# Optimization experiments

Hardware: AMD Instinct MI355X
Metric: run time of the kernel (lower is better)

The kernel has to match this reference:

```python
import jax, jax.numpy as jnp
import numpy as np

HIDDEN = 512
INPUT = 128
OUTPUT = 128
PRED_LEN = 32


def _gru_cell(h, gi, gh):
    # gi, gh: [B, 3H] pre-activations (input-side and hidden-side)
    i_r, i_z, i_n = jnp.split(gi, 3, axis=-1)
    h_r, h_z, h_n = jnp.split(gh, 3, axis=-1)
    r = jax.nn.sigmoid(i_r + h_r)
    z = jax.nn.sigmoid(i_z + h_z)
    n = jnp.tanh(i_n + r * h_n)
    return (1.0 - z) * n + z * h


def setup_inputs() -> dict:
    key = jax.random.key(0)
    ks = jax.random.split(key, 7)
    B, L = 512, 512
    s = 0.05
    return {
        "z_seq": jax.random.normal(ks[0], (B, L, INPUT), dtype=jnp.float32),
        "W_ih": jax.random.normal(ks[1], (3 * HIDDEN, INPUT), dtype=jnp.float32) * s,
        "W_hh": jax.random.normal(ks[2], (3 * HIDDEN, HIDDEN), dtype=jnp.float32) * s,
        "b_ih": jax.random.normal(ks[3], (3 * HIDDEN,), dtype=jnp.float32) * s,
        "b_hh": jax.random.normal(ks[4], (3 * HIDDEN,), dtype=jnp.float32) * s,
        "W_out": jax.random.normal(ks[5], (OUTPUT, HIDDEN), dtype=jnp.float32) * s,
        "b_out": jax.random.normal(ks[6], (OUTPUT,), dtype=jnp.float32) * s,
    }


def reference(z_seq, W_ih, W_hh, b_ih, b_hh, W_out, b_out):
    B, L, C = z_seq.shape
    h0 = jnp.zeros((B, HIDDEN), dtype=z_seq.dtype)

    # Precompute input-side pre-activations for all encode steps: [L, B, 3H]
    gi_enc = jnp.einsum('blc,gc->lbg', z_seq, W_ih) + b_ih

    def enc_step(h, gi):
        gh = h @ W_hh.T + b_hh
        return _gru_cell(h, gi, gh), None

    h_t, _ = jax.lax.scan(enc_step, h0, gi_enc)

    # Decode: input is always zeros, so input-side pre-activation is just b_ih
    gi_dec = jnp.broadcast_to(b_ih, (B, 3 * HIDDEN))

    def dec_step(h, _):
        gh = h @ W_hh.T + b_hh
        h_new = _gru_cell(h, gi_dec, gh)
        y = h_new @ W_out.T + b_out
        return h_new, y

    _, ys = jax.lax.scan(dec_step, h_t, None, length=PRED_LEN)  # [pred_len, B, O]
    return jnp.transpose(ys, (1, 0, 2))  # [B, pred_len, O]
```

## Files before the change

### kernel.cpp

```cpp
#include <hip/hip_runtime.h>

#define BATCH 512
#define SEQL  512
#define NIN   128
#define NH    512
#define NOUT  128
#define PRED  32
#define NSTEP (SEQL + PRED)

#define G_B 8
#define G_H 32
#define BT  64
#define NWG (G_B * G_H)
#define NTHREADS 256

#define OFF_WIH  24576
#define OFF_WOUT 30720
#define OFF_TR   38912
#define LDS_SH   40448

typedef short bf16x8 __attribute__((ext_vector_type(8)));
typedef float f32x4 __attribute__((ext_vector_type(4)));
typedef unsigned int u32x4 __attribute__((ext_vector_type(4)));

#define MFMA __builtin_amdgcn_mfma_f32_16x16x32_bf16

__device__ __forceinline__ unsigned short f2bf(float f) {
    unsigned int u = __float_as_uint(f);
    u = (u + 0x7fffu + ((u >> 16) & 1u)) >> 16;
    return (unsigned short)u;
}
__device__ __forceinline__ float sigm(float x) {
    x = fminf(fmaxf(x, -30.f), 30.f);
    return 1.f / (1.f + __expf(-x));
}
__device__ __forceinline__ float tanh_f(float x) {
    x = fminf(fmaxf(x, -15.f), 15.f);
    float e = __expf(2.f * x);
    return (e - 1.f) / (e + 1.f);
}

__global__ __launch_bounds__(256) void zero_kernel(unsigned short* hbuf, int* cnt)
{
    const int tid = threadIdx.x, wg = blockIdx.x;
    u32x4 z = {0, 0, 0, 0};
    char* base = (char*)hbuf + ((wg * 256 + tid) * 32);
    asm volatile("global_store_dwordx4 %0, %1, off sc1" :: "v"(base), "v"(z) : "memory");
    asm volatile("global_store_dwordx4 %0, %1, off offset:16 sc1" :: "v"(base), "v"(z) : "memory");
    if (wg == 0) {
        int zz = 0;
        asm volatile("global_store_dword %0, %1, off sc1" :: "v"(cnt + tid), "v"(zz) : "memory");
        asm volatile("global_store_dword %0, %1, off sc1" :: "v"(cnt + 256 + tid), "v"(zz) : "memory");
    }
}

__global__ __launch_bounds__(NTHREADS, 1) void gru_kernel(
    const float* __restrict__ z_seq, const float* __restrict__ W_ih,
    const float* __restrict__ W_hh, const float* __restrict__ b_ih,
    const float* __restrict__ b_hh, const float* __restrict__ W_out,
    const float* __restrict__ b_out, float* __restrict__ out,
    unsigned short* __restrict__ hbuf, int* __restrict__ cnt)
{
    __shared__ unsigned short s_w[LDS_SH];
    const int tid = threadIdx.x;
    const int wg  = blockIdx.x;
    const int bg  = wg & 7;
    const int hs  = wg >> 3;

    for (int i = tid; i < 24576; i += NTHREADS) {
        int e = i & 7, ln = (i >> 3) & 63, ks = (i >> 9) & 15, g = i >> 13;
        int unit = hs * 16 + (ln & 15);
        int k = ks * 32 + (ln >> 4) * 8 + e;
        s_w[i] = f2bf(W_hh[(g * 512 + unit) * 512 + k]);
    }
    for (int i = tid; i < 6144; i += NTHREADS) {
        int e = i & 7, ln = (i >> 3) & 63, ks = (i >> 9) & 3, g = i >> 11;
        int unit = hs * 16 + (ln & 15);
        int k = ks * 32 + (ln >> 4) * 8 + e;
        s_w[OFF_WIH + i] = f2bf(W_ih[(g * 512 + unit) * 128 + k]);
    }
    for (int i = tid; i < 8192; i += NTHREADS) {
        int e = i & 7, ln = (i >> 3) & 63, ks = i >> 9;
        int ocol = hs * 4 + (ln & 3);
        int k = ks * 32 + (ln >> 4) * 8 + e;
        s_w[OFF_WOUT + i] = f2bf(W_out[ocol * 512 + k]);
    }
    __syncthreads();

    const int lane = tid & 63;
    const int wave = tid >> 6;
    const int li   = lane & 15;
    const int kq   = lane >> 4;
    const int jg   = hs * 16 + li;

    const float bihr = b_ih[jg], bihz = b_ih[NH + jg], bihn = b_ih[2 * NH + jg];
    const float bhhr = b_hh[jg], bhhz = b_hh[NH + jg], bhhn = b_hh[2 * NH + jg];
    const float bo   = b_out[hs * 4 + (li & 3)];

    const int aRow = bg * BT + wave * 16 + li;
    const int cRow = bg * BT + wave * 16 + kq * 4;
    float hreg[4] = {0.f, 0.f, 0.f, 0.f};

    const unsigned short* fb = s_w + lane * 8;
    unsigned short* tr = s_w + OFF_TR + wave * 384;

    int* gflags = cnt + bg * 64;
    int* myFlag = gflags + hs;
    int  dead   = 0;

    f32x4 ir = {0,0,0,0}, iz = {0,0,0,0}, in = {0,0,0,0};
    {
        const float* zrow = z_seq + ((long)aRow * SEQL + 0) * NIN + kq * 8;
#pragma unroll
        for (int ks = 0; ks < 4; ++ks) {
            float4 z0 = *(const float4*)(zrow + ks * 32);
            float4 z1 = *(const float4*)(zrow + ks * 32 + 4);
            union { bf16x8 v; unsigned short u[8]; } az;
            az.u[0] = f2bf(z0.x); az.u[1] = f2bf(z0.y);
            az.u[2] = f2bf(z0.z); az.u[3] = f2bf(z0.w);
            az.u[4] = f2bf(z1.x); az.u[5] = f2bf(z1.y);
            az.u[6] = f2bf(z1.z); az.u[7] = f2bf(z1.w);
            ir = MFMA(az.v, *(const bf16x8*)(fb + OFF_WIH + ks * 512), ir, 0, 0, 0);
            iz = MFMA(az.v, *(const bf16x8*)(fb + OFF_WIH + 2048 + ks * 512), iz, 0, 0, 0);
            in = MFMA(az.v, *(const bf16x8*)(fb + OFF_WIH + 4096 + ks * 512), in, 0, 0, 0);
        }
    }

    for (int t = 0; t <= NSTEP; ++t) {
        const unsigned short* hin  = hbuf + (t & 1) * (BATCH * NH);
        unsigned short*       hout = hbuf + ((t & 1) ^ 1) * (BATCH * NH);

        const unsigned short* hrow = hin + aRow * NH + kq * 8;
        bf16x8 a[16];
#pragma unroll
        for (int ks = 0; ks < 16; ++ks)
            asm volatile("global_load_dwordx4 %0, %1, off offset:%2 sc1"
                         : "=v"(a[ks]) : "v"(hrow), "i"(ks * 64) : "memory");
        asm volatile("s_waitcnt vmcnt(0)" ::: "memory");
        __builtin_amdgcn_sched_barrier(0);

        if (t > SEQL) {
            int td = t - SEQL - 1;
            f32x4 y4 = {0, 0, 0, 0};
#pragma unroll
            for (int ks = 0; ks < 16; ++ks)
                y4 = MFMA(a[ks], *(const bf16x8*)(fb + OFF_WOUT + ks * 512), y4, 0, 0, 0);
            if (li < 4) {
#pragma unroll
                for (int q = 0; q < 4; ++q)
                    out[((long)(cRow + q) * PRED + td) * NOUT + hs * 4 + li] = y4[q] + bo;
            }
        }
        if (t == NSTEP) break;

        f32x4 hr = {0,0,0,0}, hz = {0,0,0,0}, hn = {0,0,0,0};
#pragma unroll
        for (int ks = 0; ks < 16; ++ks) {
            hr = MFMA(a[ks], *(const bf16x8*)(fb + ks * 512), hr, 0, 0, 0);
            hz = MFMA(a[ks], *(const bf16x8*)(fb + 8192 + ks * 512), hz, 0, 0, 0);
            hn = MFMA(a[ks], *(const bf16x8*)(fb + 16384 + ks * 512), hn, 0, 0, 0);
        }

#pragma unroll
        for (int q = 0; q < 4; ++q) {
            float r  = sigm(bihr + ir[q] + bhhr + hr[q]);
            float zz = sigm(bihz + iz[q] + bhhz + hz[q]);
            float nn = tanh_f(bihn + in[q] + r * (bhhn + hn[q]));
            float hq = (1.f - zz) * nn + zz * hreg[q];
            hreg[q]  = hq;
            tr[(kq * 4 + q) * 24 + li] = f2bf(hq);
        }
        asm volatile("s_waitcnt lgkmcnt(0)" ::: "memory");
        __builtin_amdgcn_sched_barrier(0);

        if (lane < 32) {
            bf16x8 hv = *(const bf16x8*)(tr + (lane >> 1) * 24 + (lane & 1) * 8);
            int grow = bg * BT + wave * 16 + (lane >> 1);
            unsigned short* hp = hout + grow * NH + hs * 16 + (lane & 1) * 8;
            asm volatile("global_store_dwordx4 %0, %1, off sc1"
                         :: "v"(hp), "v"(hv) : "memory");
        }
        asm volatile("s_waitcnt vmcnt(0)" ::: "memory");
        __syncthreads();
        if (tid == 0) {
            int v = t + 1;
            asm volatile("global_store_dword %0, %1, off sc1"
                         :: "v"(myFlag), "v"(v) : "memory");
        }

        f32x4 nir = {0,0,0,0}, niz = {0,0,0,0}, nin = {0,0,0,0};
        if (t + 1 < SEQL) {
            const float* zrow = z_seq + ((long)aRow * SEQL + (t + 1)) * NIN + kq * 8;
#pragma unroll
            for (int ks = 0; ks < 4; ++ks) {
                float4 z0 = *(const float4*)(zrow + ks * 32);
                float4 z1 = *(const float4*)(zrow + ks * 32 + 4);
                union { bf16x8 v; unsigned short u[8]; } az;
                az.u[0] = f2bf(z0.x); az.u[1] = f2bf(z0.y);
                az.u[2] = f2bf(z0.z); az.u[3] = f2bf(z0.w);
                az.u[4] = f2bf(z1.x); az.u[5] = f2bf(z1.y);
                az.u[6] = f2bf(z1.z); az.u[7] = f2bf(z1.w);
                nir = MFMA(az.v, *(const bf16x8*)(fb + OFF_WIH + ks * 512), nir, 0, 0, 0);
                niz = MFMA(az.v, *(const bf16x8*)(fb + OFF_WIH + 2048 + ks * 512), niz, 0, 0, 0);
                nin = MFMA(az.v, *(const bf16x8*)(fb + OFF_WIH + 4096 + ks * 512), nin, 0, 0, 0);
            }
        }

        const int target = t + 1;
        int bail = 0;
        if (!dead && lane == 0) {
            int patience = 4000000;
            for (;;) {
                int4 f0, f1, f2, f3, f4, f5, f6, f7;
                asm volatile(
                    "global_load_dwordx4 %0, %8, off sc1\n\t"
                    "global_load_dwordx4 %1, %8, off offset:16 sc1\n\t"
                    "global_load_dwordx4 %2, %8, off offset:32 sc1\n\t"
                    "global_load_dwordx4 %3, %8, off offset:48 sc1\n\t"
                    "global_load_dwordx4 %4, %8, off offset:64 sc1\n\t"
                    "global_load_dwordx4 %5, %8, off offset:80 sc1\n\t"
                    "global_load_dwordx4 %6, %8, off offset:96 sc1\n\t"
                    "global_load_dwordx4 %7, %8, off offset:112 sc1\n\t"
                    "s_waitcnt vmcnt(0)"
                    : "=&v"(f0), "=&v"(f1), "=&v"(f2), "=&v"(f3),
                      "=&v"(f4), "=&v"(f5), "=&v"(f6), "=&v"(f7)
                    : "v"(gflags) : "memory");
                int m0 = min(min(min(f0.x, f0.y), min(f0.z, f0.w)),
                             min(min(f1.x, f1.y), min(f1.z, f1.w)));
                int m1 = min(min(min(f2.x, f2.y), min(f2.z, f2.w)),
                             min(min(f3.x, f3.y), min(f3.z, f3.w)));
                int m2 = min(min(min(f4.x, f4.y), min(f4.z, f4.w)),
                             min(min(f5.x, f5.y), min(f5.z, f5.w)));
                int m3 = min(min(min(f6.x, f6.y), min(f6.z, f6.w)),
                             min(min(f7.x, f7.y), min(f7.z, f7.w)));
                if (min(min(m0, m1), min(m2, m3)) >= target) break;
                if (--patience == 0) { bail = 1; break; }
            }
        }
        dead |= __builtin_amdgcn_readfirstlane(bail);
        __builtin_amdgcn_sched_barrier(0);

        ir = nir; iz = niz; in = nin;
    }
}

extern "C" void kernel_launch(void* const* d_in, const int* in_sizes, int n_in,
                              void* d_out, int out_size, void* d_ws, size_t ws_size,
                              hipStream_t stream)
{
    const float* z_seq = (const float*)d_in[0];
    const float* W_ih  = (const float*)d_in[1];
    const float* W_hh  = (const float*)d_in[2];
    const float* b_ih  = (const float*)d_in[3];
    const float* b_hh  = (const float*)d_in[4];
    const float* W_out = (const float*)d_in[5];
    const float* b_out = (const float*)d_in[6];
    float* out = (float*)d_out;

    unsigned short* hbuf = (unsigned short*)d_ws;
    int* cnt = (int*)((char*)d_ws + (size_t)2 * BATCH * NH * 2);

    zero_kernel<<<dim3(64), dim3(256), 0, stream>>>(hbuf, cnt);
    gru_kernel<<<dim3(NWG), dim3(NTHREADS), 0, stream>>>(
        z_seq, W_ih, W_hh, b_ih, b_hh, W_out, b_out, out, hbuf, cnt);
}
```

Baseline: 2.818 ms.

## Replace workgroup-level step barrier with per-wave flag synchronization

```diff
diff --git a/kernel.cpp b/kernel.cpp
--- a/kernel.cpp
+++ b/kernel.cpp
@@ -51,6 +51,8 @@
         int zz = 0;
         asm volatile("global_store_dword %0, %1, off sc1" :: "v"(cnt + tid), "v"(zz) : "memory");
         asm volatile("global_store_dword %0, %1, off sc1" :: "v"(cnt + 256 + tid), "v"(zz) : "memory");
+        asm volatile("global_store_dword %0, %1, off sc1" :: "v"(cnt + 512 + tid), "v"(zz) : "memory");
+        asm volatile("global_store_dword %0, %1, off sc1" :: "v"(cnt + 768 + tid), "v"(zz) : "memory");
     }
 }
 
@@ -104,9 +106,9 @@
     const unsigned short* fb = s_w + lane * 8;
     unsigned short* tr = s_w + OFF_TR + wave * 384;
 
-    int* gflags = cnt + bg * 64;
-    int* myFlag = gflags + hs;
-    int  dead   = 0;
+    int* myFlag = cnt + ((bg * 4 + wave) << 5) + hs;
+    const int* fp = cnt + ((bg * 4 + wave) << 5) + (lane & 31);
+    int  dead  = 0;
 
     f32x4 ir = {0,0,0,0}, iz = {0,0,0,0}, in = {0,0,0,0};
     {
@@ -181,8 +183,7 @@
                          :: "v"(hp), "v"(hv) : "memory");
         }
         asm volatile("s_waitcnt vmcnt(0)" ::: "memory");
-        __syncthreads();
-        if (tid == 0) {
+        if (lane == 0) {
             int v = t + 1;
             asm volatile("global_store_dword %0, %1, off sc1"
                          :: "v"(myFlag), "v"(v) : "memory");
@@ -207,37 +208,16 @@
         }
 
         const int target = t + 1;
-        int bail = 0;
-        if (!dead && lane == 0) {
-            int patience = 4000000;
+        if (!dead) {
+            int patience = 1000000;
             for (;;) {
-                int4 f0, f1, f2, f3, f4, f5, f6, f7;
-                asm volatile(
-                    "global_load_dwordx4 %0, %8, off sc1\n\t"
-                    "global_load_dwordx4 %1, %8, off offset:16 sc1\n\t"
-                    "global_load_dwordx4 %2, %8, off offset:32 sc1\n\t"
-                    "global_load_dwordx4 %3, %8, off offset:48 sc1\n\t"
-                    "global_load_dwordx4 %4, %8, off offset:64 sc1\n\t"
-                    "global_load_dwordx4 %5, %8, off offset:80 sc1\n\t"
-                    "global_load_dwordx4 %6, %8, off offset:96 sc1\n\t"
-                    "global_load_dwordx4 %7, %8, off offset:112 sc1\n\t"
-                    "s_waitcnt vmcnt(0)"
-                    : "=&v"(f0), "=&v"(f1), "=&v"(f2), "=&v"(f3),
-                      "=&v"(f4), "=&v"(f5), "=&v"(f6), "=&v"(f7)
-                    : "v"(gflags) : "memory");
-                int m0 = min(min(min(f0.x, f0.y), min(f0.z, f0.w)),
-                             min(min(f1.x, f1.y), min(f1.z, f1.w)));
-                int m1 = min(min(min(f2.x, f2.y), min(f2.z, f2.w)),
-                             min(min(f3.x, f3.y), min(f3.z, f3.w)));
-                int m2 = min(min(min(f4.x, f4.y), min(f4.z, f4.w)),
-                             min(min(f5.x, f5.y), min(f5.z, f5.w)));
-                int m3 = min(min(min(f6.x, f6.y), min(f6.z, f6.w)),
-                             min(min(f7.x, f7.y), min(f7.z, f7.w)));
-                if (min(min(m0, m1), min(m2, m3)) >= target) break;
-                if (--patience == 0) { bail = 1; break; }
+                int f;
+                asm volatile("global_load_dword %0, %1, off sc1\n\ts_waitcnt vmcnt(0)"
+                             : "=v"(f) : "v"(fp) : "memory");
+                if (__ballot(f >= target) == ~0ull) break;
+                if (--patience == 0) { dead = 1; break; }
             }
         }
-        dead |= __builtin_amdgcn_readfirstlane(bail);
         __builtin_amdgcn_sched_barrier(0);
 
         ir = nir; iz = niz; in = nin;
```

Result: slower. 3.204 ms (+13.7%).

## Halve hidden-slice workgroups, giving each 32 hidden units and 8 output columns

Applied to the files above, without the earlier changes.

```diff
diff --git a/kernel.cpp b/kernel.cpp
--- a/kernel.cpp
+++ b/kernel.cpp
@@ -9,15 +9,17 @@
 #define NSTEP (SEQL + PRED)
 
 #define G_B 8
-#define G_H 32
+#define G_H 16
 #define BT  64
+#define UW  32
 #define NWG (G_B * G_H)
 #define NTHREADS 256
 
-#define OFF_WIH  24576
-#define OFF_WOUT 30720
-#define OFF_TR   38912
-#define LDS_SH   40448
+#define OFF_WIH   49152
+#define OFF_WOUT  61440
+#define OFF_TR    69632
+#define LDS_SHORTS 71936
+#define LDS_BYTES (LDS_SHORTS * 2)
 
 typedef short bf16x8 __attribute__((ext_vector_type(8)));
 typedef float f32x4 __attribute__((ext_vector_type(4)));
@@ -50,7 +52,6 @@
     if (wg == 0) {
         int zz = 0;
         asm volatile("global_store_dword %0, %1, off sc1" :: "v"(cnt + tid), "v"(zz) : "memory");
-        asm volatile("global_store_dword %0, %1, off sc1" :: "v"(cnt + 256 + tid), "v"(zz) : "memory");
     }
 }
 
@@ -61,27 +62,29 @@
     const float* __restrict__ b_out, float* __restrict__ out,
     unsigned short* __restrict__ hbuf, int* __restrict__ cnt)
 {
-    __shared__ unsigned short s_w[LDS_SH];
+    extern __shared__ unsigned short s_w[];
     const int tid = threadIdx.x;
     const int wg  = blockIdx.x;
     const int bg  = wg & 7;
     const int hs  = wg >> 3;
 
-    for (int i = tid; i < 24576; i += NTHREADS) {
-        int e = i & 7, ln = (i >> 3) & 63, ks = (i >> 9) & 15, g = i >> 13;
-        int unit = hs * 16 + (ln & 15);
+    for (int i = tid; i < 49152; i += NTHREADS) {
+        int e = i & 7, ln = (i >> 3) & 63, ks = (i >> 9) & 15, gu = i >> 13;
+        int g = gu >> 1, u = gu & 1;
+        int unit = hs * UW + u * 16 + (ln & 15);
         int k = ks * 32 + (ln >> 4) * 8 + e;
         s_w[i] = f2bf(W_hh[(g * 512 + unit) * 512 + k]);
     }
-    for (int i = tid; i < 6144; i += NTHREADS) {
-        int e = i & 7, ln = (i >> 3) & 63, ks = (i >> 9) & 3, g = i >> 11;
-        int unit = hs * 16 + (ln & 15);
+    for (int i = tid; i < 12288; i += NTHREADS) {
+        int e = i & 7, ln = (i >> 3) & 63, ks = (i >> 9) & 3, gu = i >> 11;
+        int g = gu >> 1, u = gu & 1;
+        int unit = hs * UW + u * 16 + (ln & 15);
         int k = ks * 32 + (ln >> 4) * 8 + e;
         s_w[OFF_WIH + i] = f2bf(W_ih[(g * 512 + unit) * 128 + k]);
     }
     for (int i = tid; i < 8192; i += NTHREADS) {
         int e = i & 7, ln = (i >> 3) & 63, ks = i >> 9;
-        int ocol = hs * 4 + (ln & 3);
+        int ocol = hs * 8 + (ln & 7);
         int k = ks * 32 + (ln >> 4) * 8 + e;
         s_w[OFF_WOUT + i] = f2bf(W_out[ocol * 512 + k]);
     }
@@ -91,24 +94,29 @@
     const int wave = tid >> 6;
     const int li   = lane & 15;
     const int kq   = lane >> 4;
-    const int jg   = hs * 16 + li;
-
-    const float bihr = b_ih[jg], bihz = b_ih[NH + jg], bihn = b_ih[2 * NH + jg];
-    const float bhhr = b_hh[jg], bhhz = b_hh[NH + jg], bhhn = b_hh[2 * NH + jg];
-    const float bo   = b_out[hs * 4 + (li & 3)];
+    const int jg0  = hs * UW + li;
+    const int jg1  = jg0 + 16;
+
+    const float bihr0 = b_ih[jg0], bihz0 = b_ih[NH + jg0], bihn0 = b_ih[2 * NH + jg0];
+    const float bihr1 = b_ih[jg1], bihz1 = b_ih[NH + jg1], bihn1 = b_ih[2 * NH + jg1];
+    const float bhhr0 = b_hh[jg0], bhhz0 = b_hh[NH + jg0], bhhn0 = b_hh[2 * NH + jg0];
+    const float bhhr1 = b_hh[jg1], bhhz1 = b_hh[NH + jg1], bhhn1 = b_hh[2 * NH + jg1];
+    const float bo    = b_out[hs * 8 + (li & 7)];
 
     const int aRow = bg * BT + wave * 16 + li;
     const int cRow = bg * BT + wave * 16 + kq * 4;
-    float hreg[4] = {0.f, 0.f, 0.f, 0.f};
-
-    const unsigned short* fb = s_w + lane * 8;
-    unsigned short* tr = s_w + OFF_TR + wave * 384;
-
-    int* gflags = cnt + bg * 64;
+    float hreg[8] = {0,0,0,0,0,0,0,0};
+
+    const unsigned short* fb  = s_w + lane * 8;
+    const unsigned short* fbI = fb + OFF_WIH;
+    unsigned short* tr = s_w + OFF_TR + wave * 576;
+
+    int* gflags = cnt + bg * 32;
     int* myFlag = gflags + hs;
     int  dead   = 0;
 
-    f32x4 ir = {0,0,0,0}, iz = {0,0,0,0}, in = {0,0,0,0};
+    f32x4 ir0 = {0,0,0,0}, iz0 = {0,0,0,0}, in0 = {0,0,0,0};
+    f32x4 ir1 = {0,0,0,0}, iz1 = {0,0,0,0}, in1 = {0,0,0,0};
     {
         const float* zrow = z_seq + ((long)aRow * SEQL + 0) * NIN + kq * 8;
 #pragma unroll
@@ -120,9 +128,12 @@
             az.u[2] = f2bf(z0.z); az.u[3] = f2bf(z0.w);
             az.u[4] = f2bf(z1.x); az.u[5] = f2bf(z1.y);
             az.u[6] = f2bf(z1.z); az.u[7] = f2bf(z1.w);
-            ir = MFMA(az.v, *(const bf16x8*)(fb + OFF_WIH + ks * 512), ir, 0, 0, 0);
-            iz = MFMA(az.v, *(const bf16x8*)(fb + OFF_WIH + 2048 + ks * 512), iz, 0, 0, 0);
-            in = MFMA(az.v, *(const bf16x8*)(fb + OFF_WIH + 4096 + ks * 512), in, 0, 0, 0);
+            ir0 = MFMA(az.v, *(const bf16x8*)(fbI + ks * 512), ir0, 0, 0, 0);
+            ir1 = MFMA(az.v, *(const bf16x8*)(fbI + 2048 + ks * 512), ir1, 0, 0, 0);
+            iz0 = MFMA(az.v, *(const bf16x8*)(fbI + 4096 + ks * 512), iz0, 0, 0, 0);
+            iz1 = MFMA(az.v, *(const bf16x8*)(fbI + 6144 + ks * 512), iz1, 0, 0, 0);
+            in0 = MFMA(az.v, *(const bf16x8*)(fbI + 8192 + ks * 512), in0, 0, 0, 0);
+            in1 = MFMA(az.v, *(const bf16x8*)(fbI + 10240 + ks * 512), in1, 0, 0, 0);
         }
     }
 
@@ -145,38 +156,49 @@
 #pragma unroll
             for (int ks = 0; ks < 16; ++ks)
                 y4 = MFMA(a[ks], *(const bf16x8*)(fb + OFF_WOUT + ks * 512), y4, 0, 0, 0);
-            if (li < 4) {
+            if (li < 8) {
 #pragma unroll
                 for (int q = 0; q < 4; ++q)
-                    out[((long)(cRow + q) * PRED + td) * NOUT + hs * 4 + li] = y4[q] + bo;
+                    out[((long)(cRow + q) * PRED + td) * NOUT + hs * 8 + li] = y4[q] + bo;
             }
         }
         if (t == NSTEP) break;
 
-        f32x4 hr = {0,0,0,0}, hz = {0,0,0,0}, hn = {0,0,0,0};
+        f32x4 hr0 = {0,0,0,0}, hz0 = {0,0,0,0}, hn0 = {0,0,0,0};
+        f32x4 hr1 = {0,0,0,0}, hz1 = {0,0,0,0}, hn1 = {0,0,0,0};
 #pragma unroll
         for (int ks = 0; ks < 16; ++ks) {
-            hr = MFMA(a[ks], *(const bf16x8*)(fb + ks * 512), hr, 0, 0, 0);
-            hz = MFMA(a[ks], *(const bf16x8*)(fb + 8192 + ks * 512), hz, 0, 0, 0);
-            hn = MFMA(a[ks], *(const bf16x8*)(fb + 16384 + ks * 512), hn, 0, 0, 0);
+            hr0 = MFMA(a[ks], *(const bf16x8*)(fb + ks * 512), hr0, 0, 0, 0);
+            hr1 = MFMA(a[ks], *(const bf16x8*)(fb + 8192 + ks * 512), hr1, 0, 0, 0);
+            hz0 = MFMA(a[ks], *(const bf16x8*)(fb + 16384 + ks * 512), hz0, 0, 0, 0);
+            hz1 = MFMA(a[ks], *(const bf16x8*)(fb + 24576 + ks * 512), hz1, 0, 0, 0);
+            hn0 = MFMA(a[ks], *(const bf16x8*)(fb + 32768 + ks * 512), hn0, 0, 0, 0);
+            hn1 = MFMA(a[ks], *(const bf16x8*)(fb + 40960 + ks * 512), hn1, 0, 0, 0);
         }
 
 #pragma unroll
         for (int q = 0; q < 4; ++q) {
-            float r  = sigm(bihr + ir[q] + bhhr + hr[q]);
-            float zz = sigm(bihz + iz[q] + bhhz + hz[q]);
-            float nn = tanh_f(bihn + in[q] + r * (bhhn + hn[q]));
-            float hq = (1.f - zz) * nn + zz * hreg[q];
-            hreg[q]  = hq;
-            tr[(kq * 4 + q) * 24 + li] = f2bf(hq);
+            float r0 = sigm(bihr0 + ir0[q] + bhhr0 + hr0[q]);
+            float z0 = sigm(bihz0 + iz0[q] + bhhz0 + hz0[q]);
+            float n0 = tanh_f(bihn0 + in0[q] + r0 * (bhhn0 + hn0[q]));
+            float h0 = (1.f - z0) * n0 + z0 * hreg[q];
+            hreg[q] = h0;
+            tr[(kq * 4 + q) * 36 + li] = f2bf(h0);
+
+            float r1 = sigm(bihr1 + ir1[q] + bhhr1 + hr1[q]);
+            float z1 = sigm(bihz1 + iz1[q] + bhhz1 + hz1[q]);
+            float n1 = tanh_f(bihn1 + in1[q] + r1 * (bhhn1 + hn1[q]));
+            float h1 = (1.f - z1) * n1 + z1 * hreg[4 + q];
+            hreg[4 + q] = h1;
+            tr[(kq * 4 + q) * 36 + 16 + li] = f2bf(h1);
         }
         asm volatile("s_waitcnt lgkmcnt(0)" ::: "memory");
         __builtin_amdgcn_sched_barrier(0);
 
-        if (lane < 32) {
-            bf16x8 hv = *(const bf16x8*)(tr + (lane >> 1) * 24 + (lane & 1) * 8);
-            int grow = bg * BT + wave * 16 + (lane >> 1);
-            unsigned short* hp = hout + grow * NH + hs * 16 + (lane & 1) * 8;
+        {
+            bf16x8 hv = *(const bf16x8*)(tr + (lane >> 2) * 36 + (lane & 3) * 8);
+            int grow = bg * BT + wave * 16 + (lane >> 2);
+            unsigned short* hp = hout + grow * NH + hs * UW + (lane & 3) * 8;
             asm volatile("global_store_dwordx4 %0, %1, off sc1"
                          :: "v"(hp), "v"(hv) : "memory");
         }
@@ -188,7 +210,8 @@
                          :: "v"(myFlag), "v"(v) : "memory");
         }
 
-        f32x4 nir = {0,0,0,0}, niz = {0,0,0,0}, nin = {0,0,0,0};
+        f32x4 nir0 = {0,0,0,0}, niz0 = {0,0,0,0}, nin0 = {0,0,0,0};
+        f32x4 nir1 = {0,0,0,0}, niz1 = {0,0,0,0}, nin1 = {0,0,0,0};
         if (t + 1 < SEQL) {
             const float* zrow = z_seq + ((long)aRow * SEQL + (t + 1)) * NIN + kq * 8;
 #pragma unroll
@@ -200,9 +223,12 @@
                 az.u[2] = f2bf(z0.z); az.u[3] = f2bf(z0.w);
                 az.u[4] = f2bf(z1.x); az.u[5] = f2bf(z1.y);
                 az.u[6] = f2bf(z1.z); az.u[7] = f2bf(z1.w);
-                nir = MFMA(az.v, *(const bf16x8*)(fb + OFF_WIH + ks * 512), nir, 0, 0, 0);
-                niz = MFMA(az.v, *(const bf16x8*)(fb + OFF_WIH + 2048 + ks * 512), niz, 0, 0, 0);
-                nin = MFMA(az.v, *(const bf16x8*)(fb + OFF_WIH + 4096 + ks * 512), nin, 0, 0, 0);
+                nir0 = MFMA(az.v, *(const bf16x8*)(fbI + ks * 512), nir0, 0, 0, 0);
+                nir1 = MFMA(az.v, *(const bf16x8*)(fbI + 2048 + ks * 512), nir1, 0, 0, 0);
+                niz0 = MFMA(az.v, *(const bf16x8*)(fbI + 4096 + ks * 512), niz0, 0, 0, 0);
+                niz1 = MFMA(az.v, *(const bf16x8*)(fbI + 6144 + ks * 512), niz1, 0, 0, 0);
+                nin0 = MFMA(az.v, *(const bf16x8*)(fbI + 8192 + ks * 512), nin0, 0, 0, 0);
+                nin1 = MFMA(az.v, *(const bf16x8*)(fbI + 10240 + ks * 512), nin1, 0, 0, 0);
             }
         }
 
@@ -211,36 +237,28 @@
         if (!dead && lane == 0) {
             int patience = 4000000;
             for (;;) {
-                int4 f0, f1, f2, f3, f4, f5, f6, f7;
+                int4 f0, f1, f2, f3;
                 asm volatile(
-                    "global_load_dwordx4 %0, %8, off sc1\n\t"
-                    "global_load_dwordx4 %1, %8, off offset:16 sc1\n\t"
-                    "global_load_dwordx4 %2, %8, off offset:32 sc1\n\t"
-                    "global_load_dwordx4 %3, %8, off offset:48 sc1\n\t"
-                    "global_load_dwordx4 %4, %8, off offset:64 sc1\n\t"
-                    "global_load_dwordx4 %5, %8, off offset:80 sc1\n\t"
-                    "global_load_dwordx4 %6, %8, off offset:96 sc1\n\t"
-                    "global_load_dwordx4 %7, %8, off offset:112 sc1\n\t"
+                    "global_load_dwordx4 %0, %4, off sc1\n\t"
+                    "global_load_dwordx4 %1, %4, off offset:16 sc1\n\t"
+                    "global_load_dwordx4 %2, %4, off offset:32 sc1\n\t"
+                    "global_load_dwordx4 %3, %4, off offset:48 sc1\n\t"
                     "s_waitcnt vmcnt(0)"
-                    : "=&v"(f0), "=&v"(f1), "=&v"(f2), "=&v"(f3),
-                      "=&v"(f4), "=&v"(f5), "=&v"(f6), "=&v"(f7)
+                    : "=&v"(f0), "=&v"(f1), "=&v"(f2), "=&v"(f3)
                     : "v"(gflags) : "memory");
                 int m0 = min(min(min(f0.x, f0.y), min(f0.z, f0.w)),
                              min(min(f1.x, f1.y), min(f1.z, f1.w)));
                 int m1 = min(min(min(f2.x, f2.y), min(f2.z, f2.w)),
                              min(min(f3.x, f3.y), min(f3.z, f3.w)));
-                int m2 = min(min(min(f4.x, f4.y), min(f4.z, f4.w)),
-                             min(min(f5.x, f5.y), min(f5.z, f5.w)));
-                int m3 = min(min(min(f6.x, f6.y), min(f6.z, f6.w)),
-                             min(min(f7.x, f7.y), min(f7.z, f7.w)));
-                if (min(min(m0, m1), min(m2, m3)) >= target) break;
+                if (min(m0, m1) >= target) break;
                 if (--patience == 0) { bail = 1; break; }
             }
         }
         dead |= __builtin_amdgcn_readfirstlane(bail);
         __builtin_amdgcn_sched_barrier(0);
 
-        ir = nir; iz = niz; in = nin;
+        ir0 = nir0; iz0 = niz0; in0 = nin0;
+        ir1 = nir1; iz1 = niz1; in1 = nin1;
     }
 }
 
@@ -261,6 +279,6 @@
     int* cnt = (int*)((char*)d_ws + (size_t)2 * BATCH * NH * 2);
 
     zero_kernel<<<dim3(64), dim3(256), 0, stream>>>(hbuf, cnt);
-    gru_kernel<<<dim3(NWG), dim3(NTHREADS), 0, stream>>>(
+    gru_kernel<<<dim3(NWG), dim3(NTHREADS), LDS_BYTES, stream>>>(
         z_seq, W_ih, W_hh, b_ih, b_hh, W_out, b_out, out, hbuf, cnt);
 }
```

New measurement: 4.158 ms. 1.48x slower.

## Split hidden units across 64 workgroups per batch group instead of 32

Applied to the files above, without the earlier changes.

```diff
diff --git a/kernel.cpp b/kernel.cpp
--- a/kernel.cpp
+++ b/kernel.cpp
@@ -9,15 +9,16 @@
 #define NSTEP (SEQL + PRED)
 
 #define G_B 8
-#define G_H 32
+#define G_H 64
 #define BT  64
+#define UW  8
 #define NWG (G_B * G_H)
 #define NTHREADS 256
 
 #define OFF_WIH  24576
 #define OFF_WOUT 30720
 #define OFF_TR   38912
-#define LDS_SH   40448
+#define LDS_SH   39680
 
 typedef short bf16x8 __attribute__((ext_vector_type(8)));
 typedef float f32x4 __attribute__((ext_vector_type(4)));
@@ -48,9 +49,8 @@
     asm volatile("global_store_dwordx4 %0, %1, off sc1" :: "v"(base), "v"(z) : "memory");
     asm volatile("global_store_dwordx4 %0, %1, off offset:16 sc1" :: "v"(base), "v"(z) : "memory");
     if (wg == 0) {
-        int zz = 0;
-        asm volatile("global_store_dword %0, %1, off sc1" :: "v"(cnt + tid), "v"(zz) : "memory");
-        asm volatile("global_store_dword %0, %1, off sc1" :: "v"(cnt + 256 + tid), "v"(zz) : "memory");
+        char* p = (char*)cnt + tid * 16;
+        asm volatile("global_store_dwordx4 %0, %1, off sc1" :: "v"(p), "v"(z) : "memory");
     }
 }
 
@@ -69,19 +69,19 @@
 
     for (int i = tid; i < 24576; i += NTHREADS) {
         int e = i & 7, ln = (i >> 3) & 63, ks = (i >> 9) & 15, g = i >> 13;
-        int unit = hs * 16 + (ln & 15);
+        int unit = hs * UW + (ln & 7);
         int k = ks * 32 + (ln >> 4) * 8 + e;
         s_w[i] = f2bf(W_hh[(g * 512 + unit) * 512 + k]);
     }
     for (int i = tid; i < 6144; i += NTHREADS) {
         int e = i & 7, ln = (i >> 3) & 63, ks = (i >> 9) & 3, g = i >> 11;
-        int unit = hs * 16 + (ln & 15);
+        int unit = hs * UW + (ln & 7);
         int k = ks * 32 + (ln >> 4) * 8 + e;
         s_w[OFF_WIH + i] = f2bf(W_ih[(g * 512 + unit) * 128 + k]);
     }
     for (int i = tid; i < 8192; i += NTHREADS) {
         int e = i & 7, ln = (i >> 3) & 63, ks = i >> 9;
-        int ocol = hs * 4 + (ln & 3);
+        int ocol = hs * 2 + (ln & 1);
         int k = ks * 32 + (ln >> 4) * 8 + e;
         s_w[OFF_WOUT + i] = f2bf(W_out[ocol * 512 + k]);
     }
@@ -91,20 +91,20 @@
     const int wave = tid >> 6;
     const int li   = lane & 15;
     const int kq   = lane >> 4;
-    const int jg   = hs * 16 + li;
+    const int jg   = hs * UW + (li & 7);
 
     const float bihr = b_ih[jg], bihz = b_ih[NH + jg], bihn = b_ih[2 * NH + jg];
     const float bhhr = b_hh[jg], bhhz = b_hh[NH + jg], bhhn = b_hh[2 * NH + jg];
-    const float bo   = b_out[hs * 4 + (li & 3)];
+    const float bo   = b_out[hs * 2 + (li & 1)];
 
     const int aRow = bg * BT + wave * 16 + li;
     const int cRow = bg * BT + wave * 16 + kq * 4;
     float hreg[4] = {0.f, 0.f, 0.f, 0.f};
 
     const unsigned short* fb = s_w + lane * 8;
-    unsigned short* tr = s_w + OFF_TR + wave * 384;
-
-    int* gflags = cnt + bg * 64;
+    unsigned short* tr = s_w + OFF_TR + wave * 192;
+
+    int* gflags = cnt + bg * 128;
     int* myFlag = gflags + hs;
     int  dead   = 0;
 
@@ -145,10 +145,10 @@
 #pragma unroll
             for (int ks = 0; ks < 16; ++ks)
                 y4 = MFMA(a[ks], *(const bf16x8*)(fb + OFF_WOUT + ks * 512), y4, 0, 0, 0);
-            if (li < 4) {
+            if (li < 2) {
 #pragma unroll
                 for (int q = 0; q < 4; ++q)
-                    out[((long)(cRow + q) * PRED + td) * NOUT + hs * 4 + li] = y4[q] + bo;
+                    out[((long)(cRow + q) * PRED + td) * NOUT + hs * 2 + li] = y4[q] + bo;
             }
         }
         if (t == NSTEP) break;
@@ -168,15 +168,15 @@
             float nn = tanh_f(bihn + in[q] + r * (bhhn + hn[q]));
             float hq = (1.f - zz) * nn + zz * hreg[q];
             hreg[q]  = hq;
-            tr[(kq * 4 + q) * 24 + li] = f2bf(hq);
+            tr[(kq * 4 + q) * 12 + (li & 7)] = f2bf(hq);
         }
         asm volatile("s_waitcnt lgkmcnt(0)" ::: "memory");
         __builtin_amdgcn_sched_barrier(0);
 
-        if (lane < 32) {
-            bf16x8 hv = *(const bf16x8*)(tr + (lane >> 1) * 24 + (lane & 1) * 8);
-            int grow = bg * BT + wave * 16 + (lane >> 1);
-            unsigned short* hp = hout + grow * NH + hs * 16 + (lane & 1) * 8;
+        if (lane < 16) {
+            bf16x8 hv = *(const bf16x8*)(tr + lane * 12);
+            int grow = bg * BT + wave * 16 + lane;
+            unsigned short* hp = hout + grow * NH + hs * UW;
             asm volatile("global_store_dwordx4 %0, %1, off sc1"
                          :: "v"(hp), "v"(hv) : "memory");
         }
@@ -212,18 +212,29 @@
             int patience = 4000000;
             for (;;) {
                 int4 f0, f1, f2, f3, f4, f5, f6, f7;
+                int4 g0, g1, g2, g3, g4, g5, g6, g7;
                 asm volatile(
-                    "global_load_dwordx4 %0, %8, off sc1\n\t"
-                    "global_load_dwordx4 %1, %8, off offset:16 sc1\n\t"
-                    "global_load_dwordx4 %2, %8, off offset:32 sc1\n\t"
-                    "global_load_dwordx4 %3, %8, off offset:48 sc1\n\t"
-                    "global_load_dwordx4 %4, %8, off offset:64 sc1\n\t"
-                    "global_load_dwordx4 %5, %8, off offset:80 sc1\n\t"
-                    "global_load_dwordx4 %6, %8, off offset:96 sc1\n\t"
-                    "global_load_dwordx4 %7, %8, off offset:112 sc1\n\t"
+                    "global_load_dwordx4 %0, %16, off sc1\n\t"
+                    "global_load_dwordx4 %1, %16, off offset:16 sc1\n\t"
+                    "global_load_dwordx4 %2, %16, off offset:32 sc1\n\t"
+                    "global_load_dwordx4 %3, %16, off offset:48 sc1\n\t"
+                    "global_load_dwordx4 %4, %16, off offset:64 sc1\n\t"
+                    "global_load_dwordx4 %5, %16, off offset:80 sc1\n\t"
+                    "global_load_dwordx4 %6, %16, off offset:96 sc1\n\t"
+                    "global_load_dwordx4 %7, %16, off offset:112 sc1\n\t"
+                    "global_load_dwordx4 %8, %16, off offset:128 sc1\n\t"
+                    "global_load_dwordx4 %9, %16, off offset:144 sc1\n\t"
+                    "global_load_dwordx4 %10, %16, off offset:160 sc1\n\t"
+                    "global_load_dwordx4 %11, %16, off offset:176 sc1\n\t"
+                    "global_load_dwordx4 %12, %16, off offset:192 sc1\n\t"
+                    "global_load_dwordx4 %13, %16, off offset:208 sc1\n\t"
+                    "global_load_dwordx4 %14, %16, off offset:224 sc1\n\t"
+                    "global_load_dwordx4 %15, %16, off offset:240 sc1\n\t"
                     "s_waitcnt vmcnt(0)"
                     : "=&v"(f0), "=&v"(f1), "=&v"(f2), "=&v"(f3),
-                      "=&v"(f4), "=&v"(f5), "=&v"(f6), "=&v"(f7)
+                      "=&v"(f4), "=&v"(f5), "=&v"(f6), "=&v"(f7),
+                      "=&v"(g0), "=&v"(g1), "=&v"(g2), "=&v"(g3),
+                      "=&v"(g4), "=&v"(g5), "=&v"(g6), "=&v"(g7)
                     : "v"(gflags) : "memory");
                 int m0 = min(min(min(f0.x, f0.y), min(f0.z, f0.w)),
                              min(min(f1.x, f1.y), min(f1.z, f1.w)));
@@ -233,7 +244,17 @@
                              min(min(f5.x, f5.y), min(f5.z, f5.w)));
                 int m3 = min(min(min(f6.x, f6.y), min(f6.z, f6.w)),
                              min(min(f7.x, f7.y), min(f7.z, f7.w)));
-                if (min(min(m0, m1), min(m2, m3)) >= target) break;
+                int m4 = min(min(min(g0.x, g0.y), min(g0.z, g0.w)),
+                             min(min(g1.x, g1.y), min(g1.z, g1.w)));
+                int m5 = min(min(min(g2.x, g2.y), min(g2.z, g2.w)),
+                             min(min(g3.x, g3.y), min(g3.z, g3.w)));
+                int m6 = min(min(min(g4.x, g4.y), min(g4.z, g4.w)),
+                             min(min(g5.x, g5.y), min(g5.z, g5.w)));
+                int m7 = min(min(min(g6.x, g6.y), min(g6.z, g6.w)),
+                             min(min(g7.x, g7.y), min(g7.z, g7.w)));
+                int m = min(min(min(m0, m1), min(m2, m3)),
+                            min(min(m4, m5), min(m6, m7)));
+                if (m >= target) break;
                 if (--patience == 0) { bail = 1; break; }
             }
         }
```

Measured after the change: 9.117 ms. 224% more time.
